# Optimization experiments

Measured on AMD Instinct MI355X. Metric: run time of the kernel, lower is better.

## Reference

```python
import jax, jax.numpy as jnp
import numpy as np

T = 5       # Newton-Schulz iterations
EPS = 1e-5


def setup_inputs() -> dict:
    key = jax.random.key(0)
    k1, k2 = jax.random.split(key)
    N, F = 500000, 128
    X = jax.random.normal(k1, (N, F), dtype=jnp.float32)
    # running_rot buffer: random orthogonal rotation (eye at init; use QR for a non-trivial one)
    M = jax.random.normal(k2, (1, F, F), dtype=jnp.float32)
    Q, _ = jnp.linalg.qr(M)
    return {"X": X, "running_rot": Q.astype(jnp.float32)}


def _whiten(X):
    # iterative_normalization_py.forward, training path, g=1 group
    x = X.T[None]                              # [g=1, d, m]
    d, m = x.shape[1], x.shape[2]
    mean = jnp.mean(x, axis=-1, keepdims=True)
    xc = x - mean                              # centered [1, d, m]
    I = jnp.eye(d, dtype=X.dtype)[None]
    # Sigma = eps*I + xc xc^T / m  (baddbmm with beta=eps, alpha=1/m)
    Sigma = EPS * I + jnp.einsum('gdm,gem->gde', xc, xc) / m
    rTr = 1.0 / jnp.trace(Sigma, axis1=1, axis2=2)[:, None, None]  # 1/tr(Sigma)
    Sn = Sigma * rTr                           # trace-normalized covariance
    P = I
    for _ in range(T):                         # P_{k+1} = 1.5 P_k - 0.5 P_k^3 Sn
        P = 1.5 * P - 0.5 * (P @ P @ P @ Sn)
    wm = P * jnp.sqrt(rTr)                     # whitening matrix = Sigma^{-1/2} (approx)
    xn = wm @ xc                               # [1, d, m]
    return xn[0].T                             # back to [N, F]


def reference(X, running_rot):
    Xn = _whiten(X)                            # [N, F]
    # X_hat = einsum('bgc,gdc->bgd', X_hat, running_rot) with g=1
    out = jnp.einsum('nc,dc->nd', Xn, running_rot[0])
    return out
```

## Files before the change

kernel.cpp:

```cpp
#include <hip/hip_runtime.h>
#include <math.h>

#define NROWS  500000
#define NCHK   7813
#define EPSV   1e-5f

typedef __bf16 bf16_t;
typedef __bf16 bf16x4 __attribute__((ext_vector_type(4)));
typedef __bf16 bf16x8 __attribute__((ext_vector_type(8)));
typedef float  f32x4  __attribute__((ext_vector_type(4)));

static const size_t WB_OFF   = 327680;
static const size_t MEAN_OFF = 360448;
static const size_t BIAS_OFF = 360960;
static const size_t CS_OFF   = 393216;
static const size_t GRAM_OFF = 1048576;

__global__ __launch_bounds__(256) void k_stats(const float* __restrict__ X,
        float* __restrict__ csPart, float* __restrict__ gramPart) {
    __shared__ bf16_t sxtT[2][8192];
    __shared__ float  scs[256][4];
    const int t    = threadIdx.x;
    const int lane = t & 63;
    const int w    = t >> 6;
    const int oct  = t >> 5;
    const int fg4  = t & 31;
    const int cl   = lane & 15;
    const int kq   = lane >> 4;
    const int G    = gridDim.x;

    f32x4 acc[2][8];
    #pragma unroll
    for (int a = 0; a < 2; a++)
        #pragma unroll
        for (int b = 0; b < 8; b++)
            acc[a][b] = (f32x4){0.f, 0.f, 0.f, 0.f};
    float cs0 = 0.f, cs1 = 0.f, cs2 = 0.f, cs3 = 0.f;

    f32x4 R[8];

    auto KF = [](int f) { return (f ^ (f >> 3)) & 7; };

    auto GLOADC = [&](int ch) {
        const size_t row0 = (size_t)ch << 6;
        #pragma unroll
        for (int i = 0; i < 8; i++) {
            const size_t row = row0 + oct * 8 + i;
            R[i] = (row < NROWS)
                 ? *reinterpret_cast<const f32x4*>(X + row * 128 + fg4 * 4)
                 : (f32x4){0.f, 0.f, 0.f, 0.f};
        }
    };
    auto DSWRITEC = [&](int buf) {
        #pragma unroll
        for (int i = 0; i < 8; i++) {
            cs0 += R[i][0]; cs1 += R[i][1]; cs2 += R[i][2]; cs3 += R[i][3];
        }
        bf16_t* S = sxtT[buf];
        #pragma unroll
        for (int j = 0; j < 4; j++) {
            const int f = fg4 * 4 + j;
            const int g = oct ^ KF(f);
            bf16x8 v;
            #pragma unroll
            for (int i = 0; i < 8; i++) v[i] = (bf16_t)R[i][j];
            *reinterpret_cast<bf16x8*>(&S[f * 64 + g * 8]) = v;
        }
    };
    auto MFMAC = [&](int buf) {
        const bf16_t* S = sxtT[buf];
        #pragma unroll
        for (int kb = 0; kb < 2; kb++) {
            const int gq = kb * 4 + kq;
            bf16x8 fa[2];
            #pragma unroll
            for (int a = 0; a < 2; a++) {
                const int f = (w * 2 + a) * 16 + cl;
                fa[a] = *reinterpret_cast<const bf16x8*>(&S[f * 64 + ((gq ^ KF(f)) << 3)]);
            }
            #pragma unroll
            for (int b = 0; b < 8; b++) {
                const int f = b * 16 + cl;
                const bf16x8 fb = *reinterpret_cast<const bf16x8*>(&S[f * 64 + ((gq ^ KF(f)) << 3)]);
                acc[0][b] = __builtin_amdgcn_mfma_f32_16x16x32_bf16(fa[0], fb, acc[0][b], 0, 0, 0);
                acc[1][b] = __builtin_amdgcn_mfma_f32_16x16x32_bf16(fa[1], fb, acc[1][b], 0, 0, 0);
            }
        }
    };

    int ch0 = blockIdx.x;
    GLOADC(ch0);
    DSWRITEC(0);
    __syncthreads();
    for (;;) {
        const int ch1 = ch0 + G;
        const bool v1 = ch1 < NCHK;
        if (v1) GLOADC(ch1);
        MFMAC(0);
        if (v1) DSWRITEC(1);
        __syncthreads();
        if (!v1) break;
        const int ch2 = ch1 + G;
        const bool v2 = ch2 < NCHK;
        if (v2) GLOADC(ch2);
        MFMAC(1);
        if (v2) DSWRITEC(0);
        __syncthreads();
        if (!v2) break;
        ch0 = ch2;
    }

    float* gp = gramPart + (size_t)blockIdx.x * 16384;
    #pragma unroll
    for (int a = 0; a < 2; a++)
        #pragma unroll
        for (int b = 0; b < 8; b++)
            #pragma unroll
            for (int r = 0; r < 4; r++) {
                const int row = (w * 2 + a) * 16 + kq * 4 + r;
                const int col = b * 16 + cl;
                gp[row * 128 + col] = acc[a][b][r];
            }
    scs[t][0] = cs0; scs[t][1] = cs1; scs[t][2] = cs2; scs[t][3] = cs3;
    __syncthreads();
    if (t < 128) {
        float s = 0.f;
        #pragma unroll
        for (int q = 0; q < 8; q++) s += scs[q * 32 + (t >> 2)][t & 3];
        csPart[(size_t)blockIdx.x * 128 + t] = s;
    }
}

__global__ __launch_bounds__(256) void k_gred(const float* __restrict__ gramPart,
        const float* __restrict__ csPart, float* __restrict__ gpart2,
        float* __restrict__ mean, int G) {
    const int t = threadIdx.x;
    const int b = blockIdx.x;
    if (b == 128) {
        if (t < 128) {
            float s = 0.f;
            int g = 0;
            for (; g + 8 <= G; g += 8) {
                float p[8];
                #pragma unroll
                for (int u = 0; u < 8; u++) p[u] = csPart[(size_t)(g + u) * 128 + t];
                s += ((p[0] + p[1]) + (p[2] + p[3])) + ((p[4] + p[5]) + (p[6] + p[7]));
            }
            for (; g < G; g++) s += csPart[(size_t)g * 128 + t];
            mean[t] = s * (1.0f / (float)NROWS);
        }
        return;
    }
    const int eblk = b >> 3, gs = b & 7;
    const int e4 = eblk * 1024 + t * 4;
    f32x4 s = (f32x4){0.f, 0.f, 0.f, 0.f};
    int g = gs;
    for (; g + 56 < G; g += 64) {
        f32x4 v[8];
        #pragma unroll
        for (int u = 0; u < 8; u++)
            v[u] = *reinterpret_cast<const f32x4*>(&gramPart[(size_t)(g + u * 8) * 16384 + e4]);
        #pragma unroll
        for (int u = 0; u < 8; u++) s += v[u];
    }
    for (; g < G; g += 8)
        s += *reinterpret_cast<const f32x4*>(&gramPart[(size_t)g * 16384 + e4]);
    *reinterpret_cast<f32x4*>(&gpart2[(size_t)gs * 16384 + e4]) = s;
}

__global__ __launch_bounds__(512) void k_ns(const float* __restrict__ gpart2,
        const float* __restrict__ mean, const float* __restrict__ Rg,
        bf16_t* __restrict__ Wb, float* __restrict__ bias) {
    __shared__ bf16_t sPh[16384], sPl[16384], sSn[16384], sTT[16384];
    const int t = threadIdx.x;
    const int w = t >> 6, lane = t & 63;
    const int cl = lane & 15, kq = lane >> 4;

    float sig[32];
    float tr = 0.f;
    #pragma unroll
    for (int i = 0; i < 32; i++) {
        const int e = t + (i << 9);
        const int r = e >> 7, c = e & 127;
        float gsum = 0.f;
        #pragma unroll
        for (int sl = 0; sl < 8; sl++) gsum += gpart2[sl * 16384 + e];
        float s = gsum * (1.0f / (float)NROWS) - mean[r] * mean[c];
        if (r == c) { s += EPSV; tr += s; }
        sig[i] = s;
    }
    float* rs = reinterpret_cast<float*>(sTT);
    rs[t] = tr;
    __syncthreads();
    #pragma unroll
    for (int off = 256; off > 0; off >>= 1) {
        if (t < off) rs[t] += rs[t + off];
        __syncthreads();
    }
    const float rTr = 1.0f / rs[0];
    __syncthreads();
    #pragma unroll
    for (int i = 0; i < 32; i++) {
        const int e = t + (i << 9);
        const int r = e >> 7, c = e & 127;
        const int ix = r * 128 + (c ^ ((r & 7) << 3));
        const float snv = sig[i] * rTr;
        sSn[ix] = (bf16_t)snv;
        const float p0 = ((r == c) ? 1.5f : 0.f) - 0.5f * snv;
        const bf16_t ph = (bf16_t)p0;
        sPh[ix] = ph;
        sPl[ix] = (bf16_t)(p0 - (float)ph);
    }
    __syncthreads();

    f32x4 acc[8];
    auto NSMM = [&](const bf16_t* __restrict__ Bm) {
        #pragma unroll
        for (int ct = 0; ct < 8; ct++) acc[ct] = (f32x4){0.f, 0.f, 0.f, 0.f};
        const int ra = w * 16 + cl;
        #pragma unroll
        for (int kb = 0; kb < 4; kb++) {
            const int k0 = kb * 32 + kq * 8;
            const int ia = ra * 128 + (k0 ^ ((ra & 7) << 3));
            const bf16x8 ah = *reinterpret_cast<const bf16x8*>(&sPh[ia]);
            const bf16x8 al = *reinterpret_cast<const bf16x8*>(&sPl[ia]);
            #pragma unroll
            for (int ct = 0; ct < 8; ct++) {
                const int rb = ct * 16 + cl;
                const bf16x8 bb = *reinterpret_cast<const bf16x8*>(
                    &Bm[rb * 128 + (k0 ^ ((rb & 7) << 3))]);
                acc[ct] = __builtin_amdgcn_mfma_f32_16x16x32_bf16(ah, bb, acc[ct], 0, 0, 0);
                acc[ct] = __builtin_amdgcn_mfma_f32_16x16x32_bf16(al, bb, acc[ct], 0, 0, 0);
            }
        }
    };
    auto WRT = [&](bf16_t* __restrict__ D) {
        #pragma unroll
        for (int ct = 0; ct < 8; ct++)
            #pragma unroll
            for (int r = 0; r < 4; r++) {
                const int ro = w * 16 + kq * 4 + r, co = ct * 16 + cl;
                D[ro * 128 + (co ^ ((ro & 7) << 3))] = (bf16_t)acc[ct][r];
            }
    };

    for (int it = 0; it < 4; it++) {
        NSMM(sSn);
        WRT(sTT);
        __syncthreads();
        NSMM(sTT);
        __syncthreads();
        WRT(sTT);
        __syncthreads();
        NSMM(sTT);
        #pragma unroll
        for (int ct = 0; ct < 8; ct++)
            #pragma unroll
            for (int r = 0; r < 4; r++) {
                const int ro = w * 16 + kq * 4 + r, co = ct * 16 + cl;
                const int ix = ro * 128 + (co ^ ((ro & 7) << 3));
                const float pold = (float)sPh[ix] + (float)sPl[ix];
                const float pn = 1.5f * pold - 0.5f * acc[ct][r];
                const bf16_t ph = (bf16_t)pn;
                sPh[ix] = ph;
                sPl[ix] = (bf16_t)(pn - (float)ph);
            }
        __syncthreads();
    }

    const float scal = sqrtf(rTr);
    #pragma unroll
    for (int ct = 0; ct < 8; ct++) acc[ct] = (f32x4){0.f, 0.f, 0.f, 0.f};
    const int ra = w * 16 + cl;
    #pragma unroll
    for (int kb = 0; kb < 4; kb++) {
        const int k0 = kb * 32 + kq * 8;
        const float4 rv0 = *reinterpret_cast<const float4*>(&Rg[ra * 128 + k0]);
        const float4 rv1 = *reinterpret_cast<const float4*>(&Rg[ra * 128 + k0 + 4]);
        const float rv[8] = {rv0.x, rv0.y, rv0.z, rv0.w, rv1.x, rv1.y, rv1.z, rv1.w};
        bf16x8 ah, al;
        #pragma unroll
        for (int j = 0; j < 8; j++) {
            ah[j] = (bf16_t)rv[j];
            al[j] = (bf16_t)(rv[j] - (float)ah[j]);
        }
        #pragma unroll
        for (int ct = 0; ct < 8; ct++) {
            const int rb = ct * 16 + cl;
            const int ib = rb * 128 + (k0 ^ ((rb & 7) << 3));
            const bf16x8 bh = *reinterpret_cast<const bf16x8*>(&sPh[ib]);
            const bf16x8 bl = *reinterpret_cast<const bf16x8*>(&sPl[ib]);
            acc[ct] = __builtin_amdgcn_mfma_f32_16x16x32_bf16(ah, bh, acc[ct], 0, 0, 0);
            acc[ct] = __builtin_amdgcn_mfma_f32_16x16x32_bf16(al, bh, acc[ct], 0, 0, 0);
            acc[ct] = __builtin_amdgcn_mfma_f32_16x16x32_bf16(ah, bl, acc[ct], 0, 0, 0);
        }
    }
    float pb[4] = {0.f, 0.f, 0.f, 0.f};
    #pragma unroll
    for (int ct = 0; ct < 8; ct++) {
        const float mv = mean[ct * 16 + cl];
        #pragma unroll
        for (int r = 0; r < 4; r++) {
            const float wv = acc[ct][r] * scal;
            Wb[(w * 16 + kq * 4 + r) * 128 + ct * 16 + cl] = (bf16_t)wv;
            pb[r] += wv * mv;
        }
    }
    #pragma unroll
    for (int r = 0; r < 4; r++) {
        float v = pb[r];
        v += __shfl_xor(v, 1);
        v += __shfl_xor(v, 2);
        v += __shfl_xor(v, 4);
        v += __shfl_xor(v, 8);
        if (cl == 0) bias[w * 16 + kq * 4 + r] = v;
    }
}

__global__ __launch_bounds__(256) void k_out(const float* __restrict__ X,
        const bf16_t* __restrict__ Wb, const float* __restrict__ bias,
        float* __restrict__ out) {
    __shared__ bf16_t sW[128][136];
    __shared__ float sBias[128];
    const int t = threadIdx.x;
    #pragma unroll
    for (int i = 0; i < 16; i++) {
        const int idx = (t + (i << 8)) << 2;
        *reinterpret_cast<bf16x4*>(&sW[idx >> 7][idx & 127]) =
            *reinterpret_cast<const bf16x4*>(&Wb[idx]);
    }
    if (t < 128) sBias[t] = bias[t];
    __syncthreads();
    const int w = t >> 6, lane = t & 63;
    const int cl = lane & 15, kq = lane >> 4;
    const int G = gridDim.x;

    float4 A0[8], A1[8];

    auto GLOAD = [&](int tl, float4 (&B)[8]) {
        const size_t rowb = (size_t)tl * 64 + w * 16;
        const bool v = rowb < NROWS;
        const float* xr = X + (rowb + cl) * 128;
        #pragma unroll
        for (int kb = 0; kb < 4; kb++) {
            B[2*kb]   = v ? *reinterpret_cast<const float4*>(xr + kb*32 + kq*8)
                          : float4{0.f,0.f,0.f,0.f};
            B[2*kb+1] = v ? *reinterpret_cast<const float4*>(xr + kb*32 + kq*8 + 4)
                          : float4{0.f,0.f,0.f,0.f};
        }
    };
    auto COMPUTE = [&](int tl, const float4 (&B)[8]) {
        const size_t rowbase = (size_t)tl * 64 + w * 16;
        if (rowbase >= NROWS) return;
        bf16x8 ah[4], al[4];
        #pragma unroll
        for (int kb = 0; kb < 4; kb++) {
            const float4 v0 = B[2*kb], v1 = B[2*kb+1];
            const float xv[8] = {v0.x, v0.y, v0.z, v0.w, v1.x, v1.y, v1.z, v1.w};
            bf16x8 h, l;
            #pragma unroll
            for (int j = 0; j < 8; j++) {
                h[j] = (bf16_t)xv[j];
                l[j] = (bf16_t)(xv[j] - (float)h[j]);
            }
            ah[kb] = h; al[kb] = l;
        }
        #pragma unroll
        for (int ct = 0; ct < 8; ct++) {
            f32x4 acc = (f32x4){0.f, 0.f, 0.f, 0.f};
            const int d = ct * 16 + cl;
            #pragma unroll
            for (int kb = 0; kb < 4; kb++) {
                const bf16x8 bf = *reinterpret_cast<const bf16x8*>(&sW[d][kb*32 + kq*8]);
                acc = __builtin_amdgcn_mfma_f32_16x16x32_bf16(al[kb], bf, acc, 0, 0, 0);
                acc = __builtin_amdgcn_mfma_f32_16x16x32_bf16(ah[kb], bf, acc, 0, 0, 0);
            }
            const float bc = sBias[d];
            #pragma unroll
            for (int r = 0; r < 4; r++)
                out[(rowbase + kq*4 + r) * 128 + d] = acc[r] - bc;
        }
    };

    int t0 = blockIdx.x;
    if (t0 >= NCHK) return;
    GLOAD(t0, A0);
    for (;;) {
        const int t1 = t0 + G;
        if (t1 < NCHK) GLOAD(t1, A1);
        COMPUTE(t0, A0);
        if (t1 >= NCHK) break;
        const int t2 = t1 + G;
        if (t2 < NCHK) GLOAD(t2, A0);
        COMPUTE(t1, A1);
        if (t2 >= NCHK) break;
        t0 = t2;
    }
}

extern "C" void kernel_launch(void* const* d_in, const int* in_sizes, int n_in,
                              void* d_out, int out_size, void* d_ws, size_t ws_size,
                              hipStream_t stream) {
    const float* X = (const float*)d_in[0];
    const float* R = (const float*)d_in[1];
    float* out = (float*)d_out;
    char* ws = (char*)d_ws;
    bf16_t* Wb      = (bf16_t*)(ws + WB_OFF);
    float*  mean    = (float*)(ws + MEAN_OFF);
    float*  bias    = (float*)(ws + BIAS_OFF);
    float*  csPart  = (float*)(ws + CS_OFF);

    int G = 512;
    size_t avail = (ws_size > GRAM_OFF) ? (ws_size - GRAM_OFF) : 0;
    if (avail < (size_t)G * 65536 + 524288) {
        size_t forG = (avail > 524288) ? (avail - 524288) : 0;
        G = (int)(forG / 65536);
        if (G < 1) G = 1;
        if (G > 512) G = 512;
    }
    float* gramPart = (float*)(ws + GRAM_OFF);
    float* gpart2   = (float*)(ws + GRAM_OFF + (size_t)G * 65536);

    k_stats<<<dim3(G), dim3(256), 0, stream>>>(X, csPart, gramPart);
    k_gred<<<dim3(129), dim3(256), 0, stream>>>(gramPart, csPart, gpart2, mean, G);
    k_ns<<<dim3(1), dim3(512), 0, stream>>>(gpart2, mean, R, Wb, bias);
    k_out<<<dim3(2048), dim3(256), 0, stream>>>(X, Wb, bias, out);
}
```

Baseline: 219.6 us.

## Fully reduce Gram partials in k_gred and launch one k_out block per tile

The Gram reduction now produces the complete 128x128 sum in k_gred: 256 blocks each cover 64 elements across 4 slices and combine them in shared memory. The single-block Newton-Schulz kernel therefore no longer sums 8 partial slabs, which shortens its serial prologue. k_out drops its persistent double-buffered grid-stride loop and launches one block per 64-row tile, issuing the X loads before staging W into LDS. In exchange, every block reloads W and the bias, and overlap now comes from block scheduling instead of explicit register prefetch.

```diff
diff --git a/kernel.cpp b/kernel.cpp
--- a/kernel.cpp
+++ b/kernel.cpp
@@ -10,6 +10,7 @@
 typedef __bf16 bf16x8 __attribute__((ext_vector_type(8)));
 typedef float  f32x4  __attribute__((ext_vector_type(4)));
 
+static const size_t GT_OFF   = 131072;
 static const size_t WB_OFF   = 327680;
 static const size_t MEAN_OFF = 360448;
 static const size_t BIAS_OFF = 360960;
@@ -132,11 +133,11 @@
 }
 
 __global__ __launch_bounds__(256) void k_gred(const float* __restrict__ gramPart,
-        const float* __restrict__ csPart, float* __restrict__ gpart2,
+        const float* __restrict__ csPart, float* __restrict__ gramTot,
         float* __restrict__ mean, int G) {
     const int t = threadIdx.x;
     const int b = blockIdx.x;
-    if (b == 128) {
+    if (b == 256) {
         if (t < 128) {
             float s = 0.f;
             int g = 0;
@@ -151,24 +152,27 @@
         }
         return;
     }
-    const int eblk = b >> 3, gs = b & 7;
-    const int e4 = eblk * 1024 + t * 4;
-    f32x4 s = (f32x4){0.f, 0.f, 0.f, 0.f};
-    int g = gs;
-    for (; g + 56 < G; g += 64) {
-        f32x4 v[8];
+    const int e  = b * 64 + (t & 63);
+    const int sl = t >> 6;
+    float s = 0.f;
+    int g = sl;
+    for (; g + 28 < G; g += 32) {
+        float v[8];
         #pragma unroll
         for (int u = 0; u < 8; u++)
-            v[u] = *reinterpret_cast<const f32x4*>(&gramPart[(size_t)(g + u * 8) * 16384 + e4]);
-        #pragma unroll
-        for (int u = 0; u < 8; u++) s += v[u];
-    }
-    for (; g < G; g += 8)
-        s += *reinterpret_cast<const f32x4*>(&gramPart[(size_t)g * 16384 + e4]);
-    *reinterpret_cast<f32x4*>(&gpart2[(size_t)gs * 16384 + e4]) = s;
+            v[u] = gramPart[(size_t)(g + 4 * u) * 16384 + e];
+        s += ((v[0] + v[1]) + (v[2] + v[3])) + ((v[4] + v[5]) + (v[6] + v[7]));
+    }
+    for (; g < G; g += 4)
+        s += gramPart[(size_t)g * 16384 + e];
+    __shared__ float red[4][64];
+    red[sl][t & 63] = s;
+    __syncthreads();
+    if (t < 64)
+        gramTot[b * 64 + t] = (red[0][t] + red[1][t]) + (red[2][t] + red[3][t]);
 }
 
-__global__ __launch_bounds__(512) void k_ns(const float* __restrict__ gpart2,
+__global__ __launch_bounds__(512) void k_ns(const float* __restrict__ gramTot,
         const float* __restrict__ mean, const float* __restrict__ Rg,
         bf16_t* __restrict__ Wb, float* __restrict__ bias) {
     __shared__ bf16_t sPh[16384], sPl[16384], sSn[16384], sTT[16384];
@@ -182,10 +186,7 @@
     for (int i = 0; i < 32; i++) {
         const int e = t + (i << 9);
         const int r = e >> 7, c = e & 127;
-        float gsum = 0.f;
-        #pragma unroll
-        for (int sl = 0; sl < 8; sl++) gsum += gpart2[sl * 16384 + e];
-        float s = gsum * (1.0f / (float)NROWS) - mean[r] * mean[c];
+        float s = gramTot[e] * (1.0f / (float)NROWS) - mean[r] * mean[c];
         if (r == c) { s += EPSV; tr += s; }
         sig[i] = s;
     }
@@ -323,6 +324,22 @@
     __shared__ bf16_t sW[128][136];
     __shared__ float sBias[128];
     const int t = threadIdx.x;
+    const int w = t >> 6, lane = t & 63;
+    const int cl = lane & 15, kq = lane >> 4;
+    const size_t rowbase = (size_t)blockIdx.x * 64 + (size_t)w * 16;
+    const bool valid = rowbase < NROWS;
+
+    float4 B[8];
+    {
+        const float* xr = X + (rowbase + cl) * 128;
+        #pragma unroll
+        for (int kb = 0; kb < 4; kb++) {
+            B[2*kb]   = valid ? *reinterpret_cast<const float4*>(xr + kb*32 + kq*8)
+                              : float4{0.f,0.f,0.f,0.f};
+            B[2*kb+1] = valid ? *reinterpret_cast<const float4*>(xr + kb*32 + kq*8 + 4)
+                              : float4{0.f,0.f,0.f,0.f};
+        }
+    }
     #pragma unroll
     for (int i = 0; i < 16; i++) {
         const int idx = (t + (i << 8)) << 2;
@@ -331,70 +348,35 @@
     }
     if (t < 128) sBias[t] = bias[t];
     __syncthreads();
-    const int w = t >> 6, lane = t & 63;
-    const int cl = lane & 15, kq = lane >> 4;
-    const int G = gridDim.x;
-
-    float4 A0[8], A1[8];
-
-    auto GLOAD = [&](int tl, float4 (&B)[8]) {
-        const size_t rowb = (size_t)tl * 64 + w * 16;
-        const bool v = rowb < NROWS;
-        const float* xr = X + (rowb + cl) * 128;
+    if (!valid) return;
+
+    bf16x8 ah[4], al[4];
+    #pragma unroll
+    for (int kb = 0; kb < 4; kb++) {
+        const float4 v0 = B[2*kb], v1 = B[2*kb+1];
+        const float xv[8] = {v0.x, v0.y, v0.z, v0.w, v1.x, v1.y, v1.z, v1.w};
+        bf16x8 h, l;
+        #pragma unroll
+        for (int j = 0; j < 8; j++) {
+            h[j] = (bf16_t)xv[j];
+            l[j] = (bf16_t)(xv[j] - (float)h[j]);
+        }
+        ah[kb] = h; al[kb] = l;
+    }
+    #pragma unroll
+    for (int ct = 0; ct < 8; ct++) {
+        f32x4 acc = (f32x4){0.f, 0.f, 0.f, 0.f};
+        const int d = ct * 16 + cl;
         #pragma unroll
         for (int kb = 0; kb < 4; kb++) {
-            B[2*kb]   = v ? *reinterpret_cast<const float4*>(xr + kb*32 + kq*8)
-                          : float4{0.f,0.f,0.f,0.f};
-            B[2*kb+1] = v ? *reinterpret_cast<const float4*>(xr + kb*32 + kq*8 + 4)
-                          : float4{0.f,0.f,0.f,0.f};
-        }
-    };
-    auto COMPUTE = [&](int tl, const float4 (&B)[8]) {
-        const size_t rowbase = (size_t)tl * 64 + w * 16;
-        if (rowbase >= NROWS) return;
-        bf16x8 ah[4], al[4];
-        #pragma unroll
-        for (int kb = 0; kb < 4; kb++) {
-            const float4 v0 = B[2*kb], v1 = B[2*kb+1];
-            const float xv[8] = {v0.x, v0.y, v0.z, v0.w, v1.x, v1.y, v1.z, v1.w};
-            bf16x8 h, l;
-            #pragma unroll
-            for (int j = 0; j < 8; j++) {
-                h[j] = (bf16_t)xv[j];
-                l[j] = (bf16_t)(xv[j] - (float)h[j]);
-            }
-            ah[kb] = h; al[kb] = l;
-        }
-        #pragma unroll
-        for (int ct = 0; ct < 8; ct++) {
-            f32x4 acc = (f32x4){0.f, 0.f, 0.f, 0.f};
-            const int d = ct * 16 + cl;
-            #pragma unroll
-            for (int kb = 0; kb < 4; kb++) {
-                const bf16x8 bf = *reinterpret_cast<const bf16x8*>(&sW[d][kb*32 + kq*8]);
-                acc = __builtin_amdgcn_mfma_f32_16x16x32_bf16(al[kb], bf, acc, 0, 0, 0);
-                acc = __builtin_amdgcn_mfma_f32_16x16x32_bf16(ah[kb], bf, acc, 0, 0, 0);
-            }
-            const float bc = sBias[d];
-            #pragma unroll
-            for (int r = 0; r < 4; r++)
-                out[(rowbase + kq*4 + r) * 128 + d] = acc[r] - bc;
-        }
-    };
-
-    int t0 = blockIdx.x;
-    if (t0 >= NCHK) return;
-    GLOAD(t0, A0);
-    for (;;) {
-        const int t1 = t0 + G;
-        if (t1 < NCHK) GLOAD(t1, A1);
-        COMPUTE(t0, A0);
-        if (t1 >= NCHK) break;
-        const int t2 = t1 + G;
-        if (t2 < NCHK) GLOAD(t2, A0);
-        COMPUTE(t1, A1);
-        if (t2 >= NCHK) break;
-        t0 = t2;
+            const bf16x8 bf = *reinterpret_cast<const bf16x8*>(&sW[d][kb*32 + kq*8]);
+            acc = __builtin_amdgcn_mfma_f32_16x16x32_bf16(al[kb], bf, acc, 0, 0, 0);
+            acc = __builtin_amdgcn_mfma_f32_16x16x32_bf16(ah[kb], bf, acc, 0, 0, 0);
+        }
+        const float bc = sBias[d];
+        #pragma unroll
+        for (int r = 0; r < 4; r++)
+            out[(rowbase + kq*4 + r) * 128 + d] = acc[r] - bc;
     }
 }
 
@@ -405,6 +387,7 @@
     const float* R = (const float*)d_in[1];
     float* out = (float*)d_out;
     char* ws = (char*)d_ws;
+    float*  gramTot = (float*)(ws + GT_OFF);
     bf16_t* Wb      = (bf16_t*)(ws + WB_OFF);
     float*  mean    = (float*)(ws + MEAN_OFF);
     float*  bias    = (float*)(ws + BIAS_OFF);
@@ -412,17 +395,15 @@
 
     int G = 512;
     size_t avail = (ws_size > GRAM_OFF) ? (ws_size - GRAM_OFF) : 0;
-    if (avail < (size_t)G * 65536 + 524288) {
-        size_t forG = (avail > 524288) ? (avail - 524288) : 0;
-        G = (int)(forG / 65536);
+    if (avail < (size_t)G * 65536) {
+        G = (int)(avail / 65536);
         if (G < 1) G = 1;
         if (G > 512) G = 512;
     }
     float* gramPart = (float*)(ws + GRAM_OFF);
-    float* gpart2   = (float*)(ws + GRAM_OFF + (size_t)G * 65536);
 
     k_stats<<<dim3(G), dim3(256), 0, stream>>>(X, csPart, gramPart);
-    k_gred<<<dim3(129), dim3(256), 0, stream>>>(gramPart, csPart, gpart2, mean, G);
-    k_ns<<<dim3(1), dim3(512), 0, stream>>>(gpart2, mean, R, Wb, bias);
-    k_out<<<dim3(2048), dim3(256), 0, stream>>>(X, Wb, bias, out);
+    k_gred<<<dim3(257), dim3(256), 0, stream>>>(gramPart, csPart, gramTot, mean, G);
+    k_ns<<<dim3(1), dim3(512), 0, stream>>>(gramTot, mean, R, Wb, bias);
+    k_out<<<dim3(NCHK), dim3(256), 0, stream>>>(X, Wb, bias, out);
 }
```

After: 222.7 us. Within noise of the previous version (+1.4%).
